# Kernel tuning notes

Measured on AMD Instinct MI355X. Metric: run time of the kernel, lower is better.

## Reference

```python
import jax, jax.numpy as jnp
import numpy as np

T, B, H, V, L = 1024, 16, 1024, 100, 3


def setup_inputs() -> dict:
    key = jax.random.key(0)
    k_x, k_e, k_w, k_b = jax.random.split(key, 4)
    x = jax.random.randint(k_x, (T, B), 0, V)                      # [T, B] token ids
    emb = jax.random.normal(k_e, (V, H), dtype=jnp.float32) * 0.1  # embedding table
    # per-layer Linear(H, 3H): stacked weights/biases (all layers have in=out=H)
    W = jax.random.normal(k_w, (L, H, 3 * H), dtype=jnp.float32) * (1.0 / np.sqrt(H))
    b = jax.random.normal(k_b, (L, 3 * H), dtype=jnp.float32) * 0.01
    return {"x": x, "emb": emb, "W": W, "b": b}


def _qrnn_layer(h, W_l, b_l):
    # h: [T, B, H] -> gates [T, B, 3H]
    g = jnp.einsum("tbh,hk->tbk", h, W_l) + b_l
    z, f, o = jnp.split(g, 3, axis=-1)
    z = jnp.tanh(z)
    f = jax.nn.sigmoid(f)
    o = jax.nn.sigmoid(o)

    def step(c, zf):
        z_t, f_t = zf
        c = f_t * z_t + (1.0 - f_t) * c  # forget-mult recurrence
        return c, c

    c0 = jnp.zeros(h.shape[1:], dtype=h.dtype)  # hidden init is None -> zeros
    _, C = jax.lax.scan(step, c0, (z, f))       # C: [T, B, H]
    return o * C


def reference(x, emb, W, b):
    h = emb[x]  # [T, B, H]
    for l in range(L):
        h = _qrnn_layer(h, W[l], b[l])
    return h[:-1]  # drop last timestep, [T-1, B, H]
```

## Files before the change

kernel.cpp:

```cpp
#include <hip/hip_runtime.h>
#include <hip/hip_bf16.h>

#define T_DIM 1024
#define B_DIM 16
#define H_DIM 1024
#define L_DIM 3
#define M_DIM (T_DIM * B_DIM)
#define N_DIM (3 * H_DIM)
#define K_DIM H_DIM
#define NC 64
#define CS 16

typedef __bf16 bf16x8 __attribute__((ext_vector_type(8)));
typedef __bf16 bf16x4 __attribute__((ext_vector_type(4)));
typedef _Float16 half4 __attribute__((ext_vector_type(4)));
typedef float f32x4 __attribute__((ext_vector_type(4)));

__device__ __forceinline__ __bf16 f2bf(float f) {
    return (__bf16)__float2bfloat16(f);
}

__device__ __forceinline__ void async_cp16(const void* g, void* lds) {
    __builtin_amdgcn_global_load_lds(
        (__attribute__((address_space(1))) void*)g,
        (__attribute__((address_space(3))) void*)lds, 16, 0, 0);
}

#define TW_BLOCKS (32 * 96 * 3)
__global__ void prep_kernel(const float* __restrict__ W, __bf16* __restrict__ Wt,
                            const int* __restrict__ x, const float4* __restrict__ emb,
                            __bf16* __restrict__ h) {
    if (blockIdx.x < TW_BLOCKS) {
        __shared__ __bf16 tile[32][33];
        const int blk = blockIdx.x;
        const int l = blk / 3072;
        const int r2 = blk % 3072;
        const int n0 = (r2 / 32) * 32, k0 = (r2 % 32) * 32;
        const int tx = threadIdx.x & 31, ty = threadIdx.x >> 5;
        const float* Wl = W + (size_t)l * K_DIM * N_DIM;
        __bf16* Wtl = Wt + (size_t)l * N_DIM * K_DIM;
#pragma unroll
        for (int q = 0; q < 4; q++) {
            int k = ty + q * 8;
            tile[k][tx] = f2bf(Wl[(size_t)(k0 + k) * N_DIM + n0 + tx]);
        }
        __syncthreads();
#pragma unroll
        for (int q = 0; q < 4; q++) {
            int n = ty + q * 8;
            Wtl[(size_t)(n0 + n) * K_DIM + k0 + tx] = tile[tx][n];
        }
    } else {
        int i = (blockIdx.x - TW_BLOCKS) * 256 + threadIdx.x;
        int row = i >> 8;
        int j = i & 255;
        int idx = x[row];
        float4 v = emb[(size_t)idx * 256 + j];
        __bf16* dst = h + (size_t)row * H_DIM + j * 4;
        dst[0] = f2bf(v.x); dst[1] = f2bf(v.y); dst[2] = f2bf(v.z); dst[3] = f2bf(v.w);
    }
}

__global__ __launch_bounds__(256, 2) void gemm_gates(
    const __bf16* __restrict__ A,
    const __bf16* __restrict__ Wt,
    const float* __restrict__ bias,
    _Float16* __restrict__ Gz, _Float16* __restrict__ Gf, _Float16* __restrict__ Go) {
    __shared__ __align__(16) __bf16 As[128 * 64];
    __shared__ __align__(16) __bf16 Bs[128 * 64];

    const int tid = threadIdx.x;
    const int wid = tid >> 6, lane = tid & 63;
    const int bm = blockIdx.x, bn = blockIdx.y;
    const int waveM = wid >> 1, waveN = wid & 1;
    const int lm = lane & 15, kg = lane >> 4;

    int roff[4], loff[4];
#pragma unroll
    for (int q = 0; q < 4; q++) {
        int cell = q * 256 + tid;
        int r = cell >> 3, s = cell & 7;
        int g = s ^ (r & 7);
        roff[q] = r * K_DIM + g * 8;
        loff[q] = (q * 256 + wid * 64) * 8;
    }

    const __bf16* Abase = A + (size_t)(bm * 128) * K_DIM;
    const __bf16* Bbase = Wt + (size_t)(bn * 128) * K_DIM;

    f32x4 acc[4][4] = {};

    for (int k0 = 0; k0 < K_DIM; k0 += 64) {
#pragma unroll
        for (int q = 0; q < 4; q++)
            async_cp16(Abase + k0 + roff[q], As + loff[q]);
#pragma unroll
        for (int q = 0; q < 4; q++)
            async_cp16(Bbase + k0 + roff[q], Bs + loff[q]);
        __syncthreads();

#pragma unroll
        for (int h = 0; h < 2; h++) {
            const int cs = ((h * 4 + kg) ^ (lane & 7)) * 8;
            bf16x8 af[4], bf[4];
#pragma unroll
            for (int i = 0; i < 4; i++)
                af[i] = *(const bf16x8*)(As + (waveM * 64 + i * 16 + lm) * 64 + cs);
#pragma unroll
            for (int j = 0; j < 4; j++)
                bf[j] = *(const bf16x8*)(Bs + (waveN * 64 + j * 16 + lm) * 64 + cs);
#pragma unroll
            for (int i = 0; i < 4; i++)
#pragma unroll
                for (int j = 0; j < 4; j++)
                    acc[i][j] = __builtin_amdgcn_mfma_f32_16x16x32_bf16(af[i], bf[j], acc[i][j], 0, 0, 0);
        }
        __syncthreads();
    }

    const int plane = bn >> 3;
    _Float16* __restrict__ P = (plane == 0) ? Gz : (plane == 1) ? Gf : Go;
#pragma unroll
    for (int i = 0; i < 4; i++) {
#pragma unroll
        for (int j = 0; j < 4; j++) {
            int ncol = bn * 128 + waveN * 64 + j * 16 + lm;
            int col = ncol & 1023;
            float bv = bias[ncol];
#pragma unroll
            for (int r = 0; r < 4; r++) {
                int mrow = bm * 128 + waveM * 64 + i * 16 + kg * 4 + r;
                float g = acc[i][j][r] + bv;
                float val;
                if (plane == 0) {
                    float e = __expf(-2.0f * fabsf(g));
                    float rc = __builtin_amdgcn_rcpf(1.0f + e);
                    val = copysignf(fmaf(-2.0f * e, rc, 1.0f), g);
                } else {
                    float e = __expf(-g);
                    val = __builtin_amdgcn_rcpf(1.0f + e);
                }
                P[(size_t)mrow * H_DIM + col] = (_Float16)val;
            }
        }
    }
}

__global__ __launch_bounds__(256, 8) void scan_pass1(
    const _Float16* __restrict__ Gz, const _Float16* __restrict__ Gf,
    float* __restrict__ cA, float* __restrict__ cM) {
    int tid = blockIdx.x * 256 + threadIdx.x;
    int ci = tid >> 12;
    int cg = tid & 4095;
    size_t base = (size_t)(ci * CS) * 16384 + (size_t)cg * 4;
    f32x4 Aacc = {0.f, 0.f, 0.f, 0.f};
    f32x4 Macc = {1.f, 1.f, 1.f, 1.f};
#pragma unroll
    for (int s = 0; s < CS; s++) {
        half4 z = *(const half4*)(Gz + base);
        half4 f = *(const half4*)(Gf + base);
#pragma unroll
        for (int k = 0; k < 4; k++) {
            float fk = (float)f[k], zk = (float)z[k];
            Aacc[k] = fk * zk + (1.f - fk) * Aacc[k];
            Macc[k] = (1.f - fk) * Macc[k];
        }
        base += 16384;
    }
    size_t idx = (size_t)ci * 16384 + (size_t)cg * 4;
    *(f32x4*)(cA + idx) = Aacc;
    *(f32x4*)(cM + idx) = Macc;
}

__global__ __launch_bounds__(256, 8) void scan_pass2(
    const float* __restrict__ cA, const float* __restrict__ cM,
    float* __restrict__ cIn) {
    int ch = blockIdx.x * 256 + threadIdx.x;
    float c = 0.f;
#pragma unroll
    for (int ci = 0; ci < NC; ci++) {
        cIn[ci * 16384 + ch] = c;
        c = cA[ci * 16384 + ch] + cM[ci * 16384 + ch] * c;
    }
}

__global__ __launch_bounds__(256, 8) void scan_pass3(
    const _Float16* __restrict__ Gz, const _Float16* __restrict__ Gf,
    const _Float16* __restrict__ Go, const float* __restrict__ cIn,
    __bf16* __restrict__ hdst, float* __restrict__ fdst, int is_last) {
    int tid = blockIdx.x * 256 + threadIdx.x;
    int ci = tid >> 12;
    int cg = tid & 4095;
    size_t base = (size_t)(ci * CS) * 16384 + (size_t)cg * 4;
    f32x4 c = *(const f32x4*)(cIn + (size_t)ci * 16384 + (size_t)cg * 4);
#pragma unroll
    for (int s = 0; s < CS; s++) {
        int t = ci * CS + s;
        half4 z = *(const half4*)(Gz + base);
        half4 f = *(const half4*)(Gf + base);
        half4 o = *(const half4*)(Go + base);
        f32x4 val;
#pragma unroll
        for (int k = 0; k < 4; k++) {
            float fk = (float)f[k];
            c[k] = fk * (float)z[k] + (1.f - fk) * c[k];
            val[k] = (float)o[k] * c[k];
        }
        if (is_last) {
            if (t < T_DIM - 1)
                *(f32x4*)(fdst + base) = val;
        } else {
            bf16x4 hv;
#pragma unroll
            for (int k = 0; k < 4; k++) hv[k] = f2bf(val[k]);
            *(bf16x4*)(hdst + base) = hv;
        }
        base += 16384;
    }
}

extern "C" void kernel_launch(void* const* d_in, const int* in_sizes, int n_in,
                              void* d_out, int out_size, void* d_ws, size_t ws_size,
                              hipStream_t stream) {
    const int* x = (const int*)d_in[0];
    const float* emb = (const float*)d_in[1];
    const float* W = (const float*)d_in[2];
    const float* b = (const float*)d_in[3];
    float* out = (float*)d_out;

    char* ws = (char*)d_ws;
    size_t need = (size_t)L_DIM * N_DIM * K_DIM * 2
                + (size_t)M_DIM * H_DIM * 2
                + 3ull * M_DIM * H_DIM * 2
                + 3ull * NC * 16384 * 4;
    if (ws_size < need) return;

    __bf16* Wt = (__bf16*)ws;     ws += (size_t)L_DIM * N_DIM * K_DIM * 2;
    __bf16* hbuf = (__bf16*)ws;   ws += (size_t)M_DIM * H_DIM * 2;
    _Float16* Gz = (_Float16*)ws; ws += (size_t)M_DIM * H_DIM * 2;
    _Float16* Gf = (_Float16*)ws; ws += (size_t)M_DIM * H_DIM * 2;
    _Float16* Go = (_Float16*)ws; ws += (size_t)M_DIM * H_DIM * 2;
    float* cA = (float*)ws;       ws += (size_t)NC * 16384 * 4;
    float* cM = (float*)ws;       ws += (size_t)NC * 16384 * 4;
    float* cIn = (float*)ws;

    prep_kernel<<<TW_BLOCKS + 16384, 256, 0, stream>>>(W, Wt, x, (const float4*)emb, hbuf);

    for (int l = 0; l < L_DIM; l++) {
        gemm_gates<<<dim3(M_DIM / 128, N_DIM / 128), 256, 0, stream>>>(
            hbuf, Wt + (size_t)l * N_DIM * K_DIM, b + (size_t)l * N_DIM, Gz, Gf, Go);
        scan_pass1<<<(NC * 4096) / 256, 256, 0, stream>>>(Gz, Gf, cA, cM);
        scan_pass2<<<16384 / 256, 256, 0, stream>>>(cA, cM, cIn);
        int last = (l == L_DIM - 1);
        scan_pass3<<<(NC * 4096) / 256, 256, 0, stream>>>(Gz, Gf, Go, cIn, hbuf, out, last);
    }
}
```

Baseline: 559.5 us.

## Fuse chunked scan passes into one cooperative kernel with grid sync

Replaces the three-kernel chunked scan (per-chunk aggregates, serial carry pass, apply pass) with a single cooperative kernel. Each thread keeps its z/f chunk in registers, writes its chunk aggregates, does a grid-wide sync, then recomputes its carry-in by folding all earlier chunk aggregates before applying the recurrence. This removes a kernel launch, the cIn buffer and the second read of Gz/Gf. In exchange it adds redundant carry work that grows with chunk index, higher register pressure, and reliance on the cooperative launch succeeding, with a two-kernel fallback if it does not.

Result: faster. 540.5 us (-3.4%).

```diff
diff --git a/kernel.cpp b/kernel.cpp
--- a/kernel.cpp
+++ b/kernel.cpp
@@ -1,5 +1,8 @@
 #include <hip/hip_runtime.h>
 #include <hip/hip_bf16.h>
+#include <hip/hip_cooperative_groups.h>
+
+namespace coop = cooperative_groups;
 
 #define T_DIM 1024
 #define B_DIM 16
@@ -146,13 +149,82 @@
     }
 }
 
+__global__ __launch_bounds__(256, 4) void scan_fused(
+    const _Float16* __restrict__ Gz, const _Float16* __restrict__ Gf,
+    const _Float16* __restrict__ Go,
+    float* __restrict__ cA, float* __restrict__ cM,
+    __bf16* __restrict__ hdst, float* __restrict__ fdst, int is_last) {
+    int tidg = blockIdx.x * 256 + threadIdx.x;
+    int ci = tidg >> 12;
+    int chg = tidg & 4095;
+    size_t base = (size_t)(ci * CS) * 16384 + (size_t)chg * 4;
+
+    half4 zs[CS], fs[CS];
+    f32x4 Aacc = {0.f, 0.f, 0.f, 0.f};
+    f32x4 Macc = {1.f, 1.f, 1.f, 1.f};
+    {
+        size_t p = base;
+#pragma unroll
+        for (int s = 0; s < CS; s++) {
+            zs[s] = *(const half4*)(Gz + p);
+            fs[s] = *(const half4*)(Gf + p);
+#pragma unroll
+            for (int k = 0; k < 4; k++) {
+                float fk = (float)fs[s][k], zk = (float)zs[s][k];
+                Aacc[k] = fk * zk + (1.f - fk) * Aacc[k];
+                Macc[k] = (1.f - fk) * Macc[k];
+            }
+            p += 16384;
+        }
+    }
+    size_t idx = (size_t)ci * 16384 + (size_t)chg * 4;
+    *(f32x4*)(cA + idx) = Aacc;
+    *(f32x4*)(cM + idx) = Macc;
+
+    __threadfence();
+    coop::this_grid().sync();
+
+    f32x4 c = {0.f, 0.f, 0.f, 0.f};
+    for (int cj = 0; cj < ci; cj++) {
+        size_t jdx = (size_t)cj * 16384 + (size_t)chg * 4;
+        f32x4 a = *(const f32x4*)(cA + jdx);
+        f32x4 m = *(const f32x4*)(cM + jdx);
+#pragma unroll
+        for (int k = 0; k < 4; k++) c[k] = a[k] + m[k] * c[k];
+    }
+
+    size_t p = base;
+#pragma unroll
+    for (int s = 0; s < CS; s++) {
+        int t = ci * CS + s;
+        half4 o = *(const half4*)(Go + p);
+        f32x4 val;
+#pragma unroll
+        for (int k = 0; k < 4; k++) {
+            float fk = (float)fs[s][k];
+            c[k] = fk * (float)zs[s][k] + (1.f - fk) * c[k];
+            val[k] = (float)o[k] * c[k];
+        }
+        if (is_last) {
+            if (t < T_DIM - 1)
+                *(f32x4*)(fdst + p) = val;
+        } else {
+            bf16x4 hv;
+#pragma unroll
+            for (int k = 0; k < 4; k++) hv[k] = f2bf(val[k]);
+            *(bf16x4*)(hdst + p) = hv;
+        }
+        p += 16384;
+    }
+}
+
 __global__ __launch_bounds__(256, 8) void scan_pass1(
     const _Float16* __restrict__ Gz, const _Float16* __restrict__ Gf,
     float* __restrict__ cA, float* __restrict__ cM) {
-    int tid = blockIdx.x * 256 + threadIdx.x;
-    int ci = tid >> 12;
-    int cg = tid & 4095;
-    size_t base = (size_t)(ci * CS) * 16384 + (size_t)cg * 4;
+    int tidg = blockIdx.x * 256 + threadIdx.x;
+    int ci = tidg >> 12;
+    int chg = tidg & 4095;
+    size_t base = (size_t)(ci * CS) * 16384 + (size_t)chg * 4;
     f32x4 Aacc = {0.f, 0.f, 0.f, 0.f};
     f32x4 Macc = {1.f, 1.f, 1.f, 1.f};
 #pragma unroll
@@ -167,38 +239,34 @@
         }
         base += 16384;
     }
-    size_t idx = (size_t)ci * 16384 + (size_t)cg * 4;
+    size_t idx = (size_t)ci * 16384 + (size_t)chg * 4;
     *(f32x4*)(cA + idx) = Aacc;
     *(f32x4*)(cM + idx) = Macc;
 }
 
-__global__ __launch_bounds__(256, 8) void scan_pass2(
+__global__ __launch_bounds__(256, 8) void scan_pass23(
+    const _Float16* __restrict__ Gz, const _Float16* __restrict__ Gf,
+    const _Float16* __restrict__ Go,
     const float* __restrict__ cA, const float* __restrict__ cM,
-    float* __restrict__ cIn) {
-    int ch = blockIdx.x * 256 + threadIdx.x;
-    float c = 0.f;
-#pragma unroll
-    for (int ci = 0; ci < NC; ci++) {
-        cIn[ci * 16384 + ch] = c;
-        c = cA[ci * 16384 + ch] + cM[ci * 16384 + ch] * c;
-    }
-}
-
-__global__ __launch_bounds__(256, 8) void scan_pass3(
-    const _Float16* __restrict__ Gz, const _Float16* __restrict__ Gf,
-    const _Float16* __restrict__ Go, const float* __restrict__ cIn,
     __bf16* __restrict__ hdst, float* __restrict__ fdst, int is_last) {
-    int tid = blockIdx.x * 256 + threadIdx.x;
-    int ci = tid >> 12;
-    int cg = tid & 4095;
-    size_t base = (size_t)(ci * CS) * 16384 + (size_t)cg * 4;
-    f32x4 c = *(const f32x4*)(cIn + (size_t)ci * 16384 + (size_t)cg * 4);
+    int tidg = blockIdx.x * 256 + threadIdx.x;
+    int ci = tidg >> 12;
+    int chg = tidg & 4095;
+    f32x4 c = {0.f, 0.f, 0.f, 0.f};
+    for (int cj = 0; cj < ci; cj++) {
+        size_t jdx = (size_t)cj * 16384 + (size_t)chg * 4;
+        f32x4 a = *(const f32x4*)(cA + jdx);
+        f32x4 m = *(const f32x4*)(cM + jdx);
+#pragma unroll
+        for (int k = 0; k < 4; k++) c[k] = a[k] + m[k] * c[k];
+    }
+    size_t p = (size_t)(ci * CS) * 16384 + (size_t)chg * 4;
 #pragma unroll
     for (int s = 0; s < CS; s++) {
         int t = ci * CS + s;
-        half4 z = *(const half4*)(Gz + base);
-        half4 f = *(const half4*)(Gf + base);
-        half4 o = *(const half4*)(Go + base);
+        half4 z = *(const half4*)(Gz + p);
+        half4 f = *(const half4*)(Gf + p);
+        half4 o = *(const half4*)(Go + p);
         f32x4 val;
 #pragma unroll
         for (int k = 0; k < 4; k++) {
@@ -208,14 +276,14 @@
         }
         if (is_last) {
             if (t < T_DIM - 1)
-                *(f32x4*)(fdst + base) = val;
+                *(f32x4*)(fdst + p) = val;
         } else {
             bf16x4 hv;
 #pragma unroll
             for (int k = 0; k < 4; k++) hv[k] = f2bf(val[k]);
-            *(bf16x4*)(hdst + base) = hv;
-        }
-        base += 16384;
+            *(bf16x4*)(hdst + p) = hv;
+        }
+        p += 16384;
     }
 }
 
@@ -232,7 +300,7 @@
     size_t need = (size_t)L_DIM * N_DIM * K_DIM * 2
                 + (size_t)M_DIM * H_DIM * 2
                 + 3ull * M_DIM * H_DIM * 2
-                + 3ull * NC * 16384 * 4;
+                + 2ull * NC * 16384 * 4;
     if (ws_size < need) return;
 
     __bf16* Wt = (__bf16*)ws;     ws += (size_t)L_DIM * N_DIM * K_DIM * 2;
@@ -241,17 +309,34 @@
     _Float16* Gf = (_Float16*)ws; ws += (size_t)M_DIM * H_DIM * 2;
     _Float16* Go = (_Float16*)ws; ws += (size_t)M_DIM * H_DIM * 2;
     float* cA = (float*)ws;       ws += (size_t)NC * 16384 * 4;
-    float* cM = (float*)ws;       ws += (size_t)NC * 16384 * 4;
-    float* cIn = (float*)ws;
+    float* cM = (float*)ws;
+
+    int blocksPerCU = 0;
+    hipError_t qe = hipOccupancyMaxActiveBlocksPerMultiprocessor(
+        &blocksPerCU, (const void*)scan_fused, 256, 0);
+    const bool use_coop = (qe == hipSuccess && blocksPerCU >= 4);
 
     prep_kernel<<<TW_BLOCKS + 16384, 256, 0, stream>>>(W, Wt, x, (const float4*)emb, hbuf);
 
     for (int l = 0; l < L_DIM; l++) {
         gemm_gates<<<dim3(M_DIM / 128, N_DIM / 128), 256, 0, stream>>>(
             hbuf, Wt + (size_t)l * N_DIM * K_DIM, b + (size_t)l * N_DIM, Gz, Gf, Go);
-        scan_pass1<<<(NC * 4096) / 256, 256, 0, stream>>>(Gz, Gf, cA, cM);
-        scan_pass2<<<16384 / 256, 256, 0, stream>>>(cA, cM, cIn);
         int last = (l == L_DIM - 1);
-        scan_pass3<<<(NC * 4096) / 256, 256, 0, stream>>>(Gz, Gf, Go, cIn, hbuf, out, last);
-    }
-}
+
+        bool launched = false;
+        if (use_coop) {
+            const _Float16* aGz = Gz; const _Float16* aGf = Gf; const _Float16* aGo = Go;
+            float* acA = cA; float* acM = cM;
+            __bf16* ah = hbuf; float* af = out;
+            void* args[] = {(void*)&aGz, (void*)&aGf, (void*)&aGo,
+                            (void*)&acA, (void*)&acM, (void*)&ah, (void*)&af, (void*)&last};
+            hipError_t e = hipLaunchCooperativeKernel((const void*)scan_fused,
+                                                      dim3(1024), dim3(256), args, 0, stream);
+            launched = (e == hipSuccess);
+        }
+        if (!launched) {
+            scan_pass1<<<1024, 256, 0, stream>>>(Gz, Gf, cA, cM);
+            scan_pass23<<<1024, 256, 0, stream>>>(Gz, Gf, Go, cA, cM, hbuf, out, last);
+        }
+    }
+}
```
